# Optimization experiments

Measured on AMD Instinct MI355X. Metric: run time of the kernel, lower is better.

Reference implementation:

```python
import jax, jax.numpy as jnp
import numpy as np

HIDDEN = 1024
HEADS = 16
HEAD_DIM = HIDDEN // HEADS
B, S = 2, 1024


def setup_inputs() -> dict:
    key = jax.random.key(0)
    ks = jax.random.split(key, 14)
    sc = 1.0 / np.sqrt(HIDDEN)
    inp = {
        "q": jax.random.normal(ks[0], (B, S, HIDDEN), jnp.float32),
        "k": jax.random.normal(ks[1], (B, S, HIDDEN), jnp.float32),
        "v": jax.random.normal(ks[2], (B, S, HIDDEN), jnp.float32),
        "mask": jax.random.randint(ks[3], (B, S), 0, 2, jnp.int32),
        "shift": jax.random.normal(ks[4], (B * HEADS, S, S), jnp.float32) * 0.1,
        "wq": jax.random.normal(ks[5], (HIDDEN, HIDDEN), jnp.float32) * sc,
        "bq": jnp.zeros((HIDDEN,), jnp.float32),
        "wk": jax.random.normal(ks[6], (HIDDEN, HIDDEN), jnp.float32) * sc,
        "bk": jnp.zeros((HIDDEN,), jnp.float32),
        "wv": jax.random.normal(ks[7], (HIDDEN, HIDDEN), jnp.float32) * sc,
        "bv": jnp.zeros((HIDDEN,), jnp.float32),
        "wo": jax.random.normal(ks[8], (HIDDEN, HIDDEN), jnp.float32) * sc,
        "bo": jnp.zeros((HIDDEN,), jnp.float32),
    }
    return inp


def _to_heads(x):
    # (B,S,Dm) -> (B*H, S, Dh), batch-major over heads (b*H + h)
    b, s, _ = x.shape
    return x.reshape(b, s, HEADS, HEAD_DIM).transpose(0, 2, 1, 3).reshape(b * HEADS, s, HEAD_DIM)


def reference(q, k, v, mask, shift, wq, bq, wk, bk, wv, bv, wo, bo):
    b, s, dm = q.shape
    qh = _to_heads(q @ wq.T + bq)
    kh = _to_heads(k @ wk.T + bk)
    vh = _to_heads(v @ wv.T + bv)
    scores = jnp.einsum("bqd,bkd->bqk", qh, kh) / jnp.float32(np.sqrt(HEAD_DIM))
    scores = scores + shift
    # faithful to torch: mask tiled head-major (h*B + b) -> outer product m_i * m_j
    m = jnp.tile(mask, (HEADS, 1))  # (H*B, S)
    attn_mask = m[:, :, None] * m[:, None, :]  # (H*B, S, S)
    scores = jnp.where(attn_mask == 0, jnp.float32(-1e9), scores)
    p = jax.nn.softmax(scores, axis=-1)
    out = jnp.einsum("bqk,bkd->bqd", p, vh)
    out = out.reshape(b, HEADS, s, HEAD_DIM).transpose(0, 2, 1, 3).reshape(b, s, dm)
    return out @ wo.T + bo
```

## Files before the change

kernel.cpp:

```cpp
#include <hip/hip_runtime.h>
#include <hip/hip_bf16.h>

#define S_LEN 1024
#define DMODEL 1024
#define N_HEADS 16
#define D_HEAD 64
#define BATCH 2
#define N_BH 32

typedef __attribute__((ext_vector_type(8))) short short8;
typedef __attribute__((ext_vector_type(4))) float f32x4;
typedef __attribute__((ext_vector_type(4))) int i32x4;

static __device__ __forceinline__ unsigned short f2bf(float x) {
    unsigned int u = __float_as_uint(x);
    return (unsigned short)((u + 0x7fffu + ((u >> 16) & 1u)) >> 16);
}

static __device__ __forceinline__ float bf2f(unsigned short h) {
    return __uint_as_float(((unsigned int)h) << 16);
}

static __device__ __forceinline__ float sum8(short8 v) {
    float s = 0.f;
#pragma unroll
    for (int j = 0; j < 8; ++j) s += bf2f((unsigned short)v[j]);
    return s;
}

template <int AMODE>
__device__ __forceinline__ void gemm_body(const void* __restrict__ Araw,
                                          const float* __restrict__ W,
                                          const float* __restrict__ bias,
                                          void* __restrict__ outp, int outmode,
                                          int n0, int j0)
{
    __shared__ unsigned short As[128 * 40];
    __shared__ unsigned short Bs[64 * 40];
    const int t = threadIdx.x;
    const int lane = t & 63, w = t >> 6;
    const int wm = w >> 1, wn = w & 1;
    const int g = lane >> 4, r = lane & 15;

    f32x4 acc[4][2];
#pragma unroll
    for (int mi = 0; mi < 4; ++mi)
#pragma unroll
        for (int ni = 0; ni < 2; ++ni)
            acc[mi][ni] = (f32x4){0.f, 0.f, 0.f, 0.f};

    for (int ks = 0; ks < DMODEL / 32; ++ks) {
        const int k0 = ks * 32;
        __syncthreads();
        if (AMODE == 0) {
            const float* A = (const float*)Araw;
#pragma unroll
            for (int i = 0; i < 4; ++i) {
                int row = (t >> 3) + i * 32;
                int quad = t & 7;
                float4 f = *reinterpret_cast<const float4*>(A + (size_t)(n0 + row) * DMODEL + k0 + quad * 4);
                ushort4 hv = { f2bf(f.x), f2bf(f.y), f2bf(f.z), f2bf(f.w) };
                *reinterpret_cast<ushort4*>(&As[row * 40 + quad * 4]) = hv;
            }
        } else {
            const unsigned short* A = (const unsigned short*)Araw;
#pragma unroll
            for (int i = 0; i < 2; ++i) {
                int row = (t >> 2) + i * 64;
                int seg = t & 3;
                short8 v8 = *reinterpret_cast<const short8*>(A + (size_t)(n0 + row) * DMODEL + k0 + seg * 8);
                *reinterpret_cast<short8*>(&As[row * 40 + seg * 8]) = v8;
            }
        }
#pragma unroll
        for (int i = 0; i < 2; ++i) {
            int row = (t >> 3) + i * 32;
            int quad = t & 7;
            float4 f = *reinterpret_cast<const float4*>(W + (size_t)(j0 + row) * DMODEL + k0 + quad * 4);
            ushort4 hv = { f2bf(f.x), f2bf(f.y), f2bf(f.z), f2bf(f.w) };
            *reinterpret_cast<ushort4*>(&Bs[row * 40 + quad * 4]) = hv;
        }
        __syncthreads();
        short8 af[4], bfr[2];
#pragma unroll
        for (int mi = 0; mi < 4; ++mi)
            af[mi] = *reinterpret_cast<const short8*>(&As[(wm * 64 + mi * 16 + r) * 40 + g * 8]);
#pragma unroll
        for (int ni = 0; ni < 2; ++ni)
            bfr[ni] = *reinterpret_cast<const short8*>(&Bs[(wn * 32 + ni * 16 + r) * 40 + g * 8]);
#pragma unroll
        for (int mi = 0; mi < 4; ++mi)
#pragma unroll
            for (int ni = 0; ni < 2; ++ni)
                acc[mi][ni] = __builtin_amdgcn_mfma_f32_16x16x32_bf16(af[mi], bfr[ni], acc[mi][ni], 0, 0, 0);
    }

#pragma unroll
    for (int mi = 0; mi < 4; ++mi) {
#pragma unroll
        for (int ni = 0; ni < 2; ++ni) {
            int col = j0 + wn * 32 + ni * 16 + r;
            float bv = bias[col];
#pragma unroll
            for (int t4 = 0; t4 < 4; ++t4) {
                int n = n0 + wm * 64 + mi * 16 + g * 4 + t4;
                float v = acc[mi][ni][t4] + bv;
                if (outmode == 2) {
                    ((float*)outp)[(size_t)n * DMODEL + col] = v;
                } else {
                    int b_ = n >> 10, s_ = n & 1023;
                    int h_ = col >> 6, dh = col & 63;
                    if (outmode == 0)
                        ((unsigned short*)outp)[((size_t)(b_ * N_HEADS + h_) * S_LEN + s_) * D_HEAD + dh] = f2bf(v);
                    else
                        ((unsigned short*)outp)[((size_t)(b_ * N_HEADS + h_) * D_HEAD + dh) * S_LEN + s_] = f2bf(v);
                }
            }
        }
    }
}

__global__ __launch_bounds__(256) void qkv_kernel(
    const float* __restrict__ qx, const float* __restrict__ kx, const float* __restrict__ vx,
    const float* __restrict__ wq, const float* __restrict__ wk, const float* __restrict__ wv,
    const float* __restrict__ bq, const float* __restrict__ bk, const float* __restrict__ bv,
    unsigned short* Qh, unsigned short* Kh, unsigned short* Vt)
{
    const int z = blockIdx.z;
    const float* A    = (z == 0) ? qx : (z == 1) ? kx : vx;
    const float* W    = (z == 0) ? wq : (z == 1) ? wk : wv;
    const float* bias = (z == 0) ? bq : (z == 1) ? bk : bv;
    void* outp = (z == 0) ? (void*)Qh : (z == 1) ? (void*)Kh : (void*)Vt;
    gemm_body<0>(A, W, bias, outp, (z == 2) ? 1 : 0, blockIdx.x * 128, blockIdx.y * 64);
}

__global__ __launch_bounds__(256) void oproj_kernel(
    const unsigned short* __restrict__ attn, const float* __restrict__ wo,
    const float* __restrict__ bo, float* out)
{
    gemm_body<1>(attn, wo, bo, (void*)out, 2, blockIdx.x * 128, blockIdx.y * 64);
}

__global__ __launch_bounds__(256) void score_kernel(
    const unsigned short* __restrict__ Qh, const unsigned short* __restrict__ Kh,
    const int* __restrict__ mask, const float* __restrict__ shift,
    unsigned short* __restrict__ Sbuf, int bh0)
{
    __shared__ union {
        struct { unsigned short As[128 * 72]; unsigned short Bs[64 * 72]; } st;
        float C[128 * 68];
    } u;
    const int f = blockIdx.x;
    const int per = gridDim.x >> 3;
    const int l = (f & 7) * per + (f >> 3);
    const int zloc = l >> 7;
    const int rem = l & 127;
    const int q0 = (rem & 7) << 7;
    const int j0 = (rem >> 3) << 6;
    const int bh = bh0 + zloc;
    const int t = threadIdx.x, lane = t & 63, w = t >> 6;
    const int wm = w >> 1, wn = w & 1, g = lane >> 4, r = lane & 15;
    const unsigned short* Qb = Qh + (size_t)bh * S_LEN * D_HEAD;
    const unsigned short* Kb = Kh + (size_t)bh * S_LEN * D_HEAD;
    unsigned short* Sl = Sbuf + (size_t)zloc * S_LEN * S_LEN;
    const int* mrow = mask + (bh & (BATCH - 1)) * S_LEN;

    const int rbase = t >> 4;
    const int colE = (t & 15) * 4;
    i32x4 mkE = *reinterpret_cast<const i32x4*>(mrow + j0 + colE);
    f32x4 sv[8];
    int mq[8];
#pragma unroll
    for (int c = 0; c < 8; ++c) {
        int row = c * 16 + rbase;
        sv[c] = *reinterpret_cast<const f32x4*>(
            shift + ((size_t)bh * S_LEN + q0 + row) * S_LEN + j0 + colE);
        mq[c] = mrow[q0 + row];
    }

    {
        int row = t >> 3, seg = t & 7;
#pragma unroll
        for (int i = 0; i < 4; ++i)
            *reinterpret_cast<short8*>(&u.st.As[(row + i * 32) * 72 + seg * 8]) =
                *reinterpret_cast<const short8*>(Qb + (size_t)(q0 + row + i * 32) * D_HEAD + seg * 8);
#pragma unroll
        for (int i = 0; i < 2; ++i)
            *reinterpret_cast<short8*>(&u.st.Bs[(row + i * 32) * 72 + seg * 8]) =
                *reinterpret_cast<const short8*>(Kb + (size_t)(j0 + row + i * 32) * D_HEAD + seg * 8);
    }
    __syncthreads();

    f32x4 acc[4][2];
#pragma unroll
    for (int mi = 0; mi < 4; ++mi)
#pragma unroll
        for (int ni = 0; ni < 2; ++ni)
            acc[mi][ni] = (f32x4){0.f, 0.f, 0.f, 0.f};

#pragma unroll
    for (int ks = 0; ks < 2; ++ks) {
        short8 af[4], bf[2];
#pragma unroll
        for (int mi = 0; mi < 4; ++mi)
            af[mi] = *reinterpret_cast<const short8*>(&u.st.As[(wm * 64 + mi * 16 + r) * 72 + ks * 32 + g * 8]);
#pragma unroll
        for (int ni = 0; ni < 2; ++ni)
            bf[ni] = *reinterpret_cast<const short8*>(&u.st.Bs[(wn * 32 + ni * 16 + r) * 72 + ks * 32 + g * 8]);
#pragma unroll
        for (int mi = 0; mi < 4; ++mi)
#pragma unroll
            for (int ni = 0; ni < 2; ++ni)
                acc[mi][ni] = __builtin_amdgcn_mfma_f32_16x16x32_bf16(af[mi], bf[ni], acc[mi][ni], 0, 0, 0);
    }
    __syncthreads();

#pragma unroll
    for (int mi = 0; mi < 4; ++mi)
#pragma unroll
        for (int ni = 0; ni < 2; ++ni)
#pragma unroll
            for (int t4 = 0; t4 < 4; ++t4)
                u.C[(wm * 64 + mi * 16 + g * 4 + t4) * 68 + wn * 32 + ni * 16 + r] = acc[mi][ni][t4];
    __syncthreads();

#pragma unroll
    for (int c = 0; c < 8; ++c) {
        int row = c * 16 + rbase;
        f32x4 cv = *reinterpret_cast<const f32x4*>(&u.C[row * 68 + colE]);
        float p0 = (mq[c] & mkE[0]) ? __expf(fmaf(cv[0], 0.125f, sv[c][0])) : 0.f;
        float p1 = (mq[c] & mkE[1]) ? __expf(fmaf(cv[1], 0.125f, sv[c][1])) : 0.f;
        float p2 = (mq[c] & mkE[2]) ? __expf(fmaf(cv[2], 0.125f, sv[c][2])) : 0.f;
        float p3 = (mq[c] & mkE[3]) ? __expf(fmaf(cv[3], 0.125f, sv[c][3])) : 0.f;
        if (mq[c] == 0) { p0 = p1 = p2 = p3 = 1.f; }
        ushort4 pk = { f2bf(p0), f2bf(p1), f2bf(p2), f2bf(p3) };
        *reinterpret_cast<ushort4*>(Sl + (size_t)(q0 + row) * S_LEN + j0 + colE) = pk;
    }
}

__global__ __launch_bounds__(256) void pv_kernel(
    const unsigned short* __restrict__ Sbuf, const unsigned short* __restrict__ Vt,
    unsigned short* __restrict__ attnbuf, int bh0)
{
    __shared__ unsigned short Ss[2][64 * 72];
    __shared__ unsigned short Vs[2][64 * 72];
    __shared__ float Lsum[64];
    const int f = blockIdx.x;
    const int per = gridDim.x >> 3;
    const int l = (f & 7) * per + (f >> 3);
    const int zloc = l >> 4;
    const int qxb = l & 15;
    const int bh = bh0 + zloc;
    const int q0 = qxb * 64;
    const int b_ = bh >> 4, h_ = bh & 15;
    const int t = threadIdx.x, lane = t & 63, w = t >> 6;
    const int wm = w >> 1, wn = w & 1, g = lane >> 4, r = lane & 15;
    const unsigned short* Sl = Sbuf + (size_t)zloc * S_LEN * S_LEN;
    const unsigned short* Vb = Vt + (size_t)bh * D_HEAD * S_LEN;
    const int srow = t >> 3, seg = t & 7;

    float rs0 = 0.f, rs1 = 0.f;
    f32x4 acc[2][2];
#pragma unroll
    for (int mi = 0; mi < 2; ++mi)
#pragma unroll
        for (int ni = 0; ni < 2; ++ni)
            acc[mi][ni] = (f32x4){0.f, 0.f, 0.f, 0.f};

    {
        short8 sv0 = *reinterpret_cast<const short8*>(Sl + (size_t)(q0 + srow) * S_LEN + seg * 8);
        short8 sv1 = *reinterpret_cast<const short8*>(Sl + (size_t)(q0 + srow + 32) * S_LEN + seg * 8);
        short8 vv0 = *reinterpret_cast<const short8*>(Vb + (size_t)srow * S_LEN + seg * 8);
        short8 vv1 = *reinterpret_cast<const short8*>(Vb + (size_t)(srow + 32) * S_LEN + seg * 8);
        *reinterpret_cast<short8*>(&Ss[0][srow * 72 + seg * 8]) = sv0;
        *reinterpret_cast<short8*>(&Ss[0][(srow + 32) * 72 + seg * 8]) = sv1;
        *reinterpret_cast<short8*>(&Vs[0][srow * 72 + seg * 8]) = vv0;
        *reinterpret_cast<short8*>(&Vs[0][(srow + 32) * 72 + seg * 8]) = vv1;
        rs0 += sum8(sv0);
        rs1 += sum8(sv1);
    }
    __syncthreads();

    for (int kt = 0; kt < 16; ++kt) {
        const int cur = kt & 1;
        short8 sv0, sv1, vv0, vv1;
        if (kt < 15) {
            const int k0 = (kt + 1) * 64;
            sv0 = *reinterpret_cast<const short8*>(Sl + (size_t)(q0 + srow) * S_LEN + k0 + seg * 8);
            sv1 = *reinterpret_cast<const short8*>(Sl + (size_t)(q0 + srow + 32) * S_LEN + k0 + seg * 8);
            vv0 = *reinterpret_cast<const short8*>(Vb + (size_t)srow * S_LEN + k0 + seg * 8);
            vv1 = *reinterpret_cast<const short8*>(Vb + (size_t)(srow + 32) * S_LEN + k0 + seg * 8);
        }
#pragma unroll
        for (int ks = 0; ks < 2; ++ks) {
            short8 af[2], bf[2];
#pragma unroll
            for (int mi = 0; mi < 2; ++mi)
                af[mi] = *reinterpret_cast<const short8*>(&Ss[cur][(wm * 32 + mi * 16 + r) * 72 + ks * 32 + g * 8]);
#pragma unroll
            for (int ni = 0; ni < 2; ++ni)
                bf[ni] = *reinterpret_cast<const short8*>(&Vs[cur][(wn * 32 + ni * 16 + r) * 72 + ks * 32 + g * 8]);
#pragma unroll
            for (int mi = 0; mi < 2; ++mi)
#pragma unroll
                for (int ni = 0; ni < 2; ++ni)
                    acc[mi][ni] = __builtin_amdgcn_mfma_f32_16x16x32_bf16(af[mi], bf[ni], acc[mi][ni], 0, 0, 0);
        }
        if (kt < 15) {
            *reinterpret_cast<short8*>(&Ss[cur ^ 1][srow * 72 + seg * 8]) = sv0;
            *reinterpret_cast<short8*>(&Ss[cur ^ 1][(srow + 32) * 72 + seg * 8]) = sv1;
            *reinterpret_cast<short8*>(&Vs[cur ^ 1][srow * 72 + seg * 8]) = vv0;
            *reinterpret_cast<short8*>(&Vs[cur ^ 1][(srow + 32) * 72 + seg * 8]) = vv1;
            rs0 += sum8(sv0);
            rs1 += sum8(sv1);
        }
        __syncthreads();
    }

    rs0 += __shfl_xor(rs0, 1); rs0 += __shfl_xor(rs0, 2); rs0 += __shfl_xor(rs0, 4);
    rs1 += __shfl_xor(rs1, 1); rs1 += __shfl_xor(rs1, 2); rs1 += __shfl_xor(rs1, 4);
    if (seg == 0) { Lsum[srow] = rs0; Lsum[srow + 32] = rs1; }
    __syncthreads();

#pragma unroll
    for (int mi = 0; mi < 2; ++mi)
#pragma unroll
        for (int ni = 0; ni < 2; ++ni)
#pragma unroll
            for (int t4 = 0; t4 < 4; ++t4) {
                int row = wm * 32 + mi * 16 + g * 4 + t4;
                int col = wn * 32 + ni * 16 + r;
                float o = acc[mi][ni][t4] / Lsum[row];
                attnbuf[((size_t)(b_ * S_LEN + q0 + row)) * DMODEL + h_ * D_HEAD + col] = f2bf(o);
            }
}

extern "C" void kernel_launch(void* const* d_in, const int* in_sizes, int n_in,
                              void* d_out, int out_size, void* d_ws, size_t ws_size,
                              hipStream_t stream)
{
    const float* q     = (const float*)d_in[0];
    const float* k     = (const float*)d_in[1];
    const float* v     = (const float*)d_in[2];
    const int*   mask  = (const int*)d_in[3];
    const float* shift = (const float*)d_in[4];
    const float* wq    = (const float*)d_in[5];
    const float* bq    = (const float*)d_in[6];
    const float* wk    = (const float*)d_in[7];
    const float* bk    = (const float*)d_in[8];
    const float* wv    = (const float*)d_in[9];
    const float* bv    = (const float*)d_in[10];
    const float* wo    = (const float*)d_in[11];
    const float* bo    = (const float*)d_in[12];
    float* out = (float*)d_out;

    const size_t nhalf = (size_t)N_BH * S_LEN * D_HEAD;
    unsigned short* Qh = (unsigned short*)d_ws;
    unsigned short* Kh = Qh + nhalf;
    unsigned short* Vt = Kh + nhalf;
    unsigned short* attnbuf = Vt + nhalf;
    unsigned short* Sbuf = attnbuf + (size_t)BATCH * S_LEN * DMODEL;

    const size_t base = 16u * 1024 * 1024;
    const size_t sbytes = (size_t)S_LEN * S_LEN * 2;
    int CH = 1;
    if (ws_size > base) {
        size_t c = (ws_size - base) / sbytes;
        CH = (c >= 32) ? 32 : (c < 1 ? 1 : (int)c);
    }

    dim3 blk(256);
    qkv_kernel<<<dim3(16, 16, 3), blk, 0, stream>>>(q, k, v, wq, wk, wv, bq, bk, bv, Qh, Kh, Vt);
    for (int bh0 = 0; bh0 < N_BH; bh0 += CH) {
        int c = (N_BH - bh0 < CH) ? (N_BH - bh0) : CH;
        score_kernel<<<dim3(128 * c), blk, 0, stream>>>(Qh, Kh, mask, shift, Sbuf, bh0);
        pv_kernel<<<dim3(16 * c), blk, 0, stream>>>(Sbuf, Vt, attnbuf, bh0);
    }
    oproj_kernel<<<dim3(16, 16), blk, 0, stream>>>(attnbuf, wo, bo, out);
}
```

Baseline: 126.2 us.

## Restructure score kernel to per-wave 16-row strips with register Q and direct K loads

```diff
diff --git a/kernel.cpp b/kernel.cpp
--- a/kernel.cpp
+++ b/kernel.cpp
@@ -146,95 +146,72 @@
     const int* __restrict__ mask, const float* __restrict__ shift,
     unsigned short* __restrict__ Sbuf, int bh0)
 {
-    __shared__ union {
-        struct { unsigned short As[128 * 72]; unsigned short Bs[64 * 72]; } st;
-        float C[128 * 68];
-    } u;
+    __shared__ unsigned short Plds[4][16][72];
     const int f = blockIdx.x;
     const int per = gridDim.x >> 3;
     const int l = (f & 7) * per + (f >> 3);
-    const int zloc = l >> 7;
-    const int rem = l & 127;
-    const int q0 = (rem & 7) << 7;
-    const int j0 = (rem >> 3) << 6;
+    const int zloc = l >> 6, qg = l & 63;
     const int bh = bh0 + zloc;
-    const int t = threadIdx.x, lane = t & 63, w = t >> 6;
-    const int wm = w >> 1, wn = w & 1, g = lane >> 4, r = lane & 15;
+    const int t = threadIdx.x, w = t >> 6, lane = t & 63;
+    const int g = lane >> 4, r = lane & 15;
+    const int q0 = qg * 16;
+    const int kstart = w * 256;
+
     const unsigned short* Qb = Qh + (size_t)bh * S_LEN * D_HEAD;
     const unsigned short* Kb = Kh + (size_t)bh * S_LEN * D_HEAD;
     unsigned short* Sl = Sbuf + (size_t)zloc * S_LEN * S_LEN;
-    const int* mrow = mask + (bh & (BATCH - 1)) * S_LEN;
-
-    const int rbase = t >> 4;
-    const int colE = (t & 15) * 4;
-    i32x4 mkE = *reinterpret_cast<const i32x4*>(mrow + j0 + colE);
-    f32x4 sv[8];
-    int mq[8];
-#pragma unroll
-    for (int c = 0; c < 8; ++c) {
-        int row = c * 16 + rbase;
-        sv[c] = *reinterpret_cast<const f32x4*>(
-            shift + ((size_t)bh * S_LEN + q0 + row) * S_LEN + j0 + colE);
-        mq[c] = mrow[q0 + row];
-    }
-
-    {
-        int row = t >> 3, seg = t & 7;
-#pragma unroll
-        for (int i = 0; i < 4; ++i)
-            *reinterpret_cast<short8*>(&u.st.As[(row + i * 32) * 72 + seg * 8]) =
-                *reinterpret_cast<const short8*>(Qb + (size_t)(q0 + row + i * 32) * D_HEAD + seg * 8);
-#pragma unroll
-        for (int i = 0; i < 2; ++i)
-            *reinterpret_cast<short8*>(&u.st.Bs[(row + i * 32) * 72 + seg * 8]) =
-                *reinterpret_cast<const short8*>(Kb + (size_t)(j0 + row + i * 32) * D_HEAD + seg * 8);
-    }
-    __syncthreads();
-
-    f32x4 acc[4][2];
-#pragma unroll
-    for (int mi = 0; mi < 4; ++mi)
-#pragma unroll
-        for (int ni = 0; ni < 2; ++ni)
-            acc[mi][ni] = (f32x4){0.f, 0.f, 0.f, 0.f};
-
-#pragma unroll
-    for (int ks = 0; ks < 2; ++ks) {
-        short8 af[4], bf[2];
-#pragma unroll
-        for (int mi = 0; mi < 4; ++mi)
-            af[mi] = *reinterpret_cast<const short8*>(&u.st.As[(wm * 64 + mi * 16 + r) * 72 + ks * 32 + g * 8]);
-#pragma unroll
-        for (int ni = 0; ni < 2; ++ni)
-            bf[ni] = *reinterpret_cast<const short8*>(&u.st.Bs[(wn * 32 + ni * 16 + r) * 72 + ks * 32 + g * 8]);
-#pragma unroll
-        for (int mi = 0; mi < 4; ++mi)
-#pragma unroll
-            for (int ni = 0; ni < 2; ++ni)
-                acc[mi][ni] = __builtin_amdgcn_mfma_f32_16x16x32_bf16(af[mi], bf[ni], acc[mi][ni], 0, 0, 0);
-    }
-    __syncthreads();
-
-#pragma unroll
-    for (int mi = 0; mi < 4; ++mi)
-#pragma unroll
-        for (int ni = 0; ni < 2; ++ni)
-#pragma unroll
-            for (int t4 = 0; t4 < 4; ++t4)
-                u.C[(wm * 64 + mi * 16 + g * 4 + t4) * 68 + wn * 32 + ni * 16 + r] = acc[mi][ni][t4];
-    __syncthreads();
-
-#pragma unroll
-    for (int c = 0; c < 8; ++c) {
-        int row = c * 16 + rbase;
-        f32x4 cv = *reinterpret_cast<const f32x4*>(&u.C[row * 68 + colE]);
-        float p0 = (mq[c] & mkE[0]) ? __expf(fmaf(cv[0], 0.125f, sv[c][0])) : 0.f;
-        float p1 = (mq[c] & mkE[1]) ? __expf(fmaf(cv[1], 0.125f, sv[c][1])) : 0.f;
-        float p2 = (mq[c] & mkE[2]) ? __expf(fmaf(cv[2], 0.125f, sv[c][2])) : 0.f;
-        float p3 = (mq[c] & mkE[3]) ? __expf(fmaf(cv[3], 0.125f, sv[c][3])) : 0.f;
-        if (mq[c] == 0) { p0 = p1 = p2 = p3 = 1.f; }
-        ushort4 pk = { f2bf(p0), f2bf(p1), f2bf(p2), f2bf(p3) };
-        *reinterpret_cast<ushort4*>(Sl + (size_t)(q0 + row) * S_LEN + j0 + colE) = pk;
+    const float* shb = shift + (size_t)bh * S_LEN * S_LEN;
+    const int* mp = mask + (bh & (BATCH - 1)) * S_LEN;
+
+    short8 qf0 = *reinterpret_cast<const short8*>(&Qb[(size_t)(q0 + r) * D_HEAD + g * 8]);
+    short8 qf1 = *reinterpret_cast<const short8*>(&Qb[(size_t)(q0 + r) * D_HEAD + 32 + g * 8]);
+    const int mq = mp[q0 + r];
+    const float* shp = shb + (size_t)(q0 + r) * S_LEN + kstart;
+
+    f32x4 shA[4], shB[4];
+#pragma unroll
+    for (int fn = 0; fn < 4; ++fn) {
+        shA[fn] = *reinterpret_cast<const f32x4*>(shp + fn * 16 + g * 4);
+        shB[fn] = *reinterpret_cast<const f32x4*>(shp + 64 + fn * 16 + g * 4);
+    }
+
+#pragma unroll
+    for (int kt = 0; kt < 4; ++kt) {
+        const int kbase = kstart + kt * 64;
+        const bool useA = (kt & 1) == 0;
+
+#pragma unroll
+        for (int fn = 0; fn < 4; ++fn) {
+            short8 kv0 = *reinterpret_cast<const short8*>(&Kb[(size_t)(kbase + fn * 16 + r) * D_HEAD + g * 8]);
+            short8 kv1 = *reinterpret_cast<const short8*>(&Kb[(size_t)(kbase + fn * 16 + r) * D_HEAD + 32 + g * 8]);
+            f32x4 a = (f32x4){0.f, 0.f, 0.f, 0.f};
+            a = __builtin_amdgcn_mfma_f32_16x16x32_bf16(kv0, qf0, a, 0, 0, 0);
+            a = __builtin_amdgcn_mfma_f32_16x16x32_bf16(kv1, qf1, a, 0, 0, 0);
+            f32x4 shv = useA ? shA[fn] : shB[fn];
+            i32x4 mk = *reinterpret_cast<const i32x4*>(mp + kbase + fn * 16 + g * 4);
+            float p0 = (mq & mk[0]) ? __expf(fmaf(a[0], 0.125f, shv[0])) : 0.f;
+            float p1 = (mq & mk[1]) ? __expf(fmaf(a[1], 0.125f, shv[1])) : 0.f;
+            float p2 = (mq & mk[2]) ? __expf(fmaf(a[2], 0.125f, shv[2])) : 0.f;
+            float p3 = (mq & mk[3]) ? __expf(fmaf(a[3], 0.125f, shv[3])) : 0.f;
+            if (mq == 0) { p0 = p1 = p2 = p3 = 1.f; }
+            ushort4 pk = { f2bf(p0), f2bf(p1), f2bf(p2), f2bf(p3) };
+            *reinterpret_cast<ushort4*>(&Plds[w][r][fn * 16 + g * 4]) = pk;
+        }
+
+        if (kt < 2) {
+#pragma unroll
+            for (int fn = 0; fn < 4; ++fn) {
+                f32x4 nv = *reinterpret_cast<const f32x4*>(shp + (kt + 2) * 64 + fn * 16 + g * 4);
+                if (useA) shA[fn] = nv; else shB[fn] = nv;
+            }
+        }
+
+        asm volatile("s_waitcnt lgkmcnt(0)" ::: "memory");
+        __builtin_amdgcn_sched_barrier(0);
+        short8 pf0 = *reinterpret_cast<const short8*>(&Plds[w][r][g * 8]);
+        short8 pf1 = *reinterpret_cast<const short8*>(&Plds[w][r][32 + g * 8]);
+        *reinterpret_cast<short8*>(Sl + (size_t)(q0 + r) * S_LEN + kbase + g * 8) = pf0;
+        *reinterpret_cast<short8*>(Sl + (size_t)(q0 + r) * S_LEN + kbase + 32 + g * 8) = pf1;
     }
 }
 
@@ -373,7 +350,7 @@
     qkv_kernel<<<dim3(16, 16, 3), blk, 0, stream>>>(q, k, v, wq, wk, wv, bq, bk, bv, Qh, Kh, Vt);
     for (int bh0 = 0; bh0 < N_BH; bh0 += CH) {
         int c = (N_BH - bh0 < CH) ? (N_BH - bh0) : CH;
-        score_kernel<<<dim3(128 * c), blk, 0, stream>>>(Qh, Kh, mask, shift, Sbuf, bh0);
+        score_kernel<<<dim3(64 * c), blk, 0, stream>>>(Qh, Kh, mask, shift, Sbuf, bh0);
         pv_kernel<<<dim3(16 * c), blk, 0, stream>>>(Sbuf, Vt, attnbuf, bh0);
     }
     oproj_kernel<<<dim3(16, 16), blk, 0, stream>>>(attnbuf, wo, bo, out);
```

After: 155.6 us. 23.4% more time.
